# Performance work log

Hardware: AMD Instinct MI355X
Metric: run time of the kernel (lower is better)

The kernel has to match this reference:

```python
import jax, jax.numpy as jnp
import numpy as np

EPS = 1e-8
NUM_GCN_LAYERS = 2


def _cos(a, b):
    # cosine similarity along last axis, torch.nn.CosineSimilarity semantics
    num = jnp.sum(a * b, axis=-1)
    den = jnp.maximum(jnp.linalg.norm(a, axis=-1) * jnp.linalg.norm(b, axis=-1), EPS)
    return num / den


def _masked_mean(x, mask):
    # x: [..., L, D], mask: [..., L]
    s = jnp.sum(x * mask[..., None], axis=-2)
    d = jnp.maximum(jnp.sum(mask, axis=-1, keepdims=True), 1.0)
    return s / d


def setup_inputs() -> dict:
    key = jax.random.key(0)
    ks = jax.random.split(key, 12)
    B, C, L, D, P, OM, OE, R = 32, 16, 128, 768, 196, 10, 10, 36
    return {
        "mention_text_feature": jax.random.normal(ks[0], (B, L, D), jnp.float32),
        "mention_text_mask": jnp.ones((B, L), jnp.float32),
        "mention_start_pos": jax.random.randint(ks[1], (B,), 0, L),
        "mention_end_pos": jax.random.randint(ks[2], (B,), 0, L),
        "mention_image_feature": jax.random.normal(ks[3], (B, P, D), jnp.float32),
        "mention_object_feature": jax.random.normal(ks[4], (B, OM, R, D), jnp.float32),
        "mention_object_score": jax.random.uniform(ks[5], (B, OM), jnp.float32, 0.1, 1.0),
        "entity_text_feature": jax.random.normal(ks[6], (B, C, L, D), jnp.float32),
        "entity_text_mask": jnp.ones((B, C, L), jnp.float32),
        "entity_image_feature": jax.random.normal(ks[7], (B, C, P, D), jnp.float32),
        "entity_object_feature": jax.random.normal(ks[8], (B, C, OE, R, D), jnp.float32),
        "entity_object_score": jax.random.uniform(ks[9], (B, C, OE), jnp.float32, 0.1, 1.0),
        "miet_similarity": jax.random.normal(ks[10], (B, C), jnp.float32),
        "mtei_similarity": jax.random.normal(ks[11], (B, C), jnp.float32),
    }


def _forward(mtf, mtm, msp, mep, mif, mof, mos, etf, etm, eif, eof, eos, miet, mtei):
    B, L, D = mtf.shape
    C = etf.shape[1]

    # ---- VertexEncoder ----
    v_mt = _masked_mean(mtf, mtm)      # [B, D] mention text vertex
    v_mi = jnp.mean(mif, axis=-2)      # [B, D] mention image vertex
    v_et = _masked_mean(etf, etm)      # [B, C, D] entity text vertex
    v_ei = jnp.mean(eif, axis=-2)      # [B, C, D] entity image vertex

    # ---- EdgeEncoder ----
    # mention final repr: mean of start/end token features (span boundary repr)
    start = jnp.take_along_axis(mtf, msp[:, None, None], axis=1)[:, 0]  # [B, D]
    end = jnp.take_along_axis(mtf, mep[:, None, None], axis=1)[:, 0]    # [B, D]
    m_span = 0.5 * (start + end)
    mtet = _cos(m_span[:, None, :], etf[:, :, 0])  # [B, C] vs entity CLS token

    # miei: the original double python loop over (i, j) object pairs is a
    # weighted average of pairwise cosine sims -> one fused einsum pass.
    m = jnp.mean(mof, axis=-2)         # [B, OM, D]
    e = jnp.mean(eof, axis=-2)         # [B, C, OE, D]
    mn = m / jnp.maximum(jnp.linalg.norm(m, axis=-1, keepdims=True), EPS)
    en = e / jnp.maximum(jnp.linalg.norm(e, axis=-1, keepdims=True), EPS)
    cos_ij = jnp.einsum('bid,bcjd->bcij', mn, en)          # [B, C, OM, OE]
    w = mos[:, None, :, None] * eos[:, :, None, :]          # [B, C, OM, OE]
    miei = jnp.sum(cos_ij * w, axis=(2, 3)) / jnp.sum(w, axis=(2, 3))  # [B, C]

    # ---- GCN layers ----
    edges = [jnp.broadcast_to(x[:, :, None], (B, C, D)) for x in (mtet, mtei, miet, miei)]
    vertexes = [v_mt, v_mi, v_et, v_ei]
    vertex_graph = [[(0, 2), (1, 3)], [(2, 2), (3, 3)], [(0, 0), (2, 1)], [(1, 0), (3, 1)]]
    edge_graph = [(0, 2), (0, 3), (1, 2), (1, 3)]

    def conv_v(edge, v, mention_like):
        msg = edge * (v[:, None, :] if v.ndim == 2 else v)  # [B, C, D]
        return jnp.mean(msg, axis=1) if mention_like else msg

    def conv_e(u, v):
        u2 = u[:, None, :] if u.ndim == 2 else u
        v2 = v[:, None, :] if v.ndim == 2 else v
        return u2 * v2  # [B, C, D]

    for _ in range(NUM_GCN_LAYERS):
        new_v = []
        for k, nbrs in enumerate(vertex_graph):
            mention_like = k < 2  # vertexes 0,1 are [B,D]; 2,3 are [B,C,D]
            acc = conv_v(edges[nbrs[0][0]], vertexes[nbrs[0][1]], mention_like)
            acc = acc + conv_v(edges[nbrs[1][0]], vertexes[nbrs[1][1]], mention_like)
            new_v.append(acc)
        new_e = [conv_e(vertexes[ui], vertexes[vi]) for ui, vi in edge_graph]
        vertexes, edges = new_v, new_e

    mention, entity = vertexes[0], vertexes[2]
    return _cos(mention[:, None, :], entity)  # [B, C]


def reference(mention_text_feature, mention_text_mask, mention_start_pos, mention_end_pos, mention_image_feature, mention_object_feature, mention_object_score, entity_text_feature, entity_text_mask, entity_image_feature, entity_object_feature, entity_object_score, miet_similarity, mtei_similarity):
    return _forward(mention_text_feature, mention_text_mask, mention_start_pos, mention_end_pos, mention_image_feature, mention_object_feature, mention_object_score, entity_text_feature, entity_text_mask, entity_image_feature, entity_object_feature, entity_object_score, miet_similarity, mtei_similarity)
```

## Files before the change

### kernel.cpp

```cpp
#include <hip/hip_runtime.h>

#define EPSF 1e-8f

#define B_  32
#define C_  16
#define L_  128
#define D_  768
#define D4_ 192
#define P_  196
#define OM_ 10
#define OE_ 10
#define R_  36

__device__ __forceinline__ float4 f4add(float4 a, float4 b){
  return make_float4(a.x+b.x, a.y+b.y, a.z+b.z, a.w+b.w);
}
__device__ __forceinline__ float4 f4scale(float4 a, float s){
  return make_float4(a.x*s, a.y*s, a.z*s, a.w*s);
}
__device__ __forceinline__ float f4dot(float4 a, float4 b){
  return a.x*b.x + a.y*b.y + a.z*b.z + a.w*b.w;
}
__device__ __forceinline__ float wave_sum(float v){
  #pragma unroll
  for (int off = 32; off > 0; off >>= 1) v += __shfl_down(v, off);
  return v;
}

__global__ __launch_bounds__(192)
void means_k(const float* __restrict__ eif, const float* __restrict__ etf,
             const float* __restrict__ mof, const float* __restrict__ mif,
             const float* __restrict__ mtf,
             const float* __restrict__ etm, const float* __restrict__ mtm,
             float* __restrict__ part_eif, float* __restrict__ part_etf,
             float* __restrict__ part_mof, float* __restrict__ part_mif,
             float* __restrict__ part_mtf, float* __restrict__ msum)
{
  int blk = blockIdx.x;
  const float* in; const float* mask = nullptr;
  float* part; float* ms = nullptr;
  int ROWS, CH, RPC;
  if (blk < 3584)      { in = eif; part = part_eif; ROWS = 196; CH = 7; RPC = 28; }
  else if (blk < 5632) { blk -= 3584; in = etf; mask = etm; ms = msum + 128;
                         part = part_etf; ROWS = 128; CH = 4; RPC = 32; }
  else if (blk < 6272) { blk -= 5632; in = mof; part = part_mof; ROWS = 36; CH = 2; RPC = 18; }
  else if (blk < 6496) { blk -= 6272; in = mif; part = part_mif; ROWS = 196; CH = 7; RPC = 28; }
  else                 { blk -= 6496; in = mtf; mask = mtm; ms = msum;
                         part = part_mtf; ROWS = 128; CH = 4; RPC = 32; }

  int g = blk / CH, ch = blk - g * CH;
  int r0 = ch * RPC;
  int r1 = r0 + RPC; if (r1 > ROWS) r1 = ROWS;
  int t = threadIdx.x;
  const float4* inp = (const float4*)in + (size_t)g * ROWS * D4_;
  float4 acc = make_float4(0.f, 0.f, 0.f, 0.f);
  if (mask) {
    const float* mrow = mask + (size_t)g * ROWS;
    float msacc = 0.f;
    #pragma unroll 4
    for (int r = r0; r < r1; ++r) {
      float w = mrow[r];
      float4 v = inp[(size_t)r * D4_ + t];
      acc.x += v.x * w; acc.y += v.y * w; acc.z += v.z * w; acc.w += v.w * w;
      msacc += w;
    }
    if (t == 0) ms[blk] = msacc;
  } else {
    #pragma unroll 4
    for (int r = r0; r < r1; ++r)
      acc = f4add(acc, inp[(size_t)r * D4_ + t]);
  }
  ((float4*)part)[(size_t)blk * D4_ + t] = acc;
}

__device__ __forceinline__ void combine_body(const float* __restrict__ part,
                                             const float* __restrict__ msum,
                                             float* __restrict__ out,
                                             int secblk, int CH, float invn)
{
  int idx = secblk * 256 + threadIdx.x;
  int g = idx / D4_, t = idx - g * D4_;
  const float4* pp = (const float4*)part + (size_t)(g * CH) * D4_ + t;
  float4 acc = make_float4(0.f, 0.f, 0.f, 0.f);
  for (int ch = 0; ch < CH; ++ch) acc = f4add(acc, pp[(size_t)ch * D4_]);
  float scale;
  if (msum) {
    float s = 0.f;
    for (int ch = 0; ch < CH; ++ch) s += msum[g * CH + ch];
    scale = 1.f / fmaxf(s, 1.f);
  } else scale = invn;
  ((float4*)out)[idx] = f4scale(acc, scale);
}

__global__ __launch_bounds__(256)
void combine_k(const float* __restrict__ part_eif, const float* __restrict__ part_etf,
               const float* __restrict__ part_mof, const float* __restrict__ part_mif,
               const float* __restrict__ part_mtf, const float* __restrict__ msum,
               const float* __restrict__ etf, const float* __restrict__ mtf,
               const int* __restrict__ msp, const int* __restrict__ mep,
               const float* __restrict__ mos,
               float* __restrict__ v_ei, float* __restrict__ v_et,
               float* __restrict__ m_mean, float* __restrict__ v_mi,
               float* __restrict__ v_mt, float* __restrict__ q,
               float* __restrict__ mtet)
{
  int blk = blockIdx.x;
  if (blk < 384)       { combine_body(part_eif, nullptr, v_ei, blk, 7, 1.f/196.f); return; }
  else if (blk < 768)  { combine_body(part_etf, msum + 128, v_et, blk - 384, 4, 0.f); return; }
  else if (blk < 1008) { combine_body(part_mof, nullptr, m_mean, blk - 768, 2, 1.f/36.f); return; }
  else if (blk < 1032) { combine_body(part_mif, nullptr, v_mi, blk - 1008, 7, 1.f/196.f); return; }
  else if (blk < 1056) { combine_body(part_mtf, msum, v_mt, blk - 1032, 4, 0.f); return; }
  else if (blk < 1136) {
    int w = (blk - 1056) * 4 + (threadIdx.x >> 6);
    int lane = threadIdx.x & 63;
    const float4* pm = (const float4*)part_mof + (size_t)(w * 2) * D4_;
    const float inv36 = 1.f / 36.f;
    float n = 0.f;
    #pragma unroll
    for (int k = 0; k < 3; ++k) {
      float4 v = f4scale(f4add(pm[lane + 64*k], pm[(size_t)D4_ + lane + 64*k]), inv36);
      n += f4dot(v, v);
    }
    n = wave_sum(n);
    if (lane == 0) q[w] = mos[w] / fmaxf(sqrtf(n), EPSF);
    return;
  } else {
    int w = (blk - 1136) * 4 + (threadIdx.x >> 6);
    int lane = threadIdx.x & 63;
    int b = w >> 4;
    const float4* ecls = (const float4*)etf + (size_t)w * L_ * D4_;
    const float4* mb   = (const float4*)mtf + (size_t)b * L_ * D4_;
    int sp = msp[b], ep = mep[b];
    float dt = 0.f, na = 0.f, nb = 0.f;
    #pragma unroll
    for (int k = 0; k < 3; ++k) {
      float4 a = f4scale(f4add(mb[(size_t)sp * D4_ + lane + 64*k],
                               mb[(size_t)ep * D4_ + lane + 64*k]), 0.5f);
      float4 e = ecls[lane + 64*k];
      dt += f4dot(a, e); na += f4dot(a, a); nb += f4dot(e, e);
    }
    dt = wave_sum(dt); na = wave_sum(na); nb = wave_sum(nb);
    if (lane == 0) mtet[w] = dt / fmaxf(sqrtf(na) * sqrtf(nb), EPSF);
  }
}

__global__ __launch_bounds__(128)
void eof_dot_k(const float* __restrict__ eof, const float* __restrict__ m_mean,
               const float* __restrict__ q, const float* __restrict__ eos,
               float* __restrict__ p)
{
  int blk = blockIdx.x;
  int bc = blk / 5, jp = blk - bc * 5;
  int b = bc / C_;
  int wave = threadIdx.x >> 6, lane = threadIdx.x & 63;
  int j = jp * 2 + wave;
  size_t g = (size_t)bc * OE_ + j;
  const float4* ep = (const float4*)eof + g * R_ * D4_;
  float4 a0 = make_float4(0,0,0,0), a1 = a0, a2 = a0;
  #pragma unroll 4
  for (int r = 0; r < R_; ++r) {
    const float4* row = ep + (size_t)r * D4_;
    a0 = f4add(a0, row[lane]);
    a1 = f4add(a1, row[lane + 64]);
    a2 = f4add(a2, row[lane + 128]);
  }
  const float inv36 = 1.f / 36.f;
  a0 = f4scale(a0, inv36); a1 = f4scale(a1, inv36); a2 = f4scale(a2, inv36);
  float nrm = f4dot(a0, a0) + f4dot(a1, a1) + f4dot(a2, a2);
  float s = 0.f;
  const float4* mp = (const float4*)m_mean + (size_t)b * OM_ * D4_;
  #pragma unroll
  for (int i = 0; i < OM_; ++i) {
    const float4* mr = mp + (size_t)i * D4_;
    float di = f4dot(a0, mr[lane]) + f4dot(a1, mr[lane + 64]) + f4dot(a2, mr[lane + 128]);
    s += q[b * OM_ + i] * di;
  }
  s = wave_sum(s); nrm = wave_sum(nrm);
  if (lane == 0) {
    float einv = 1.f / fmaxf(sqrtf(nrm), EPSF);
    p[g] = eos[g] * s * einv;
  }
}

__global__ __launch_bounds__(256)
void tail_k(const float* __restrict__ p, const float* __restrict__ mos,
            const float* __restrict__ eos,
            const float* __restrict__ v_mt, const float* __restrict__ v_mi,
            const float* __restrict__ v_et, const float* __restrict__ v_ei,
            const float* __restrict__ mtet, const float* __restrict__ mtei,
            const float* __restrict__ miet,
            float* __restrict__ out)
{
  __shared__ float sh_e0[C_], sh_e1[C_], sh_e2[C_], sh_e3[C_];
  __shared__ float4 sh_m4[D4_], sh_s4[D4_];
  int b = blockIdx.x, tid = threadIdx.x;

  if (tid < C_) {
    int bc = b * C_ + tid;
    float num = 0.f, se = 0.f, sm = 0.f;
    #pragma unroll
    for (int j = 0; j < OE_; ++j) { num += p[bc * OE_ + j]; se += eos[bc * OE_ + j]; }
    #pragma unroll
    for (int i = 0; i < OM_; ++i) sm += mos[b * OM_ + i];
    sh_e3[tid] = num / (sm * se);
    sh_e0[tid] = mtet[bc];
    sh_e1[tid] = mtei[bc];
    sh_e2[tid] = miet[bc];
  }
  __syncthreads();

  const float invC = 1.f / (float)C_;
  for (int d = tid; d < D_; d += 256) {
    float vmt = v_mt[b * D_ + d], vmi = v_mi[b * D_ + d];
    float nv0 = 0.f, nv1 = 0.f, macc = 0.f;
    #pragma unroll
    for (int c = 0; c < C_; ++c) {
      int bc = b * C_ + c;
      float et = v_et[(size_t)bc * D_ + d];
      float ei = v_ei[(size_t)bc * D_ + d];
      float e0 = sh_e0[c], e1 = sh_e1[c], e2 = sh_e2[c], e3 = sh_e3[c];
      nv0 += e0 * et + e1 * ei;
      nv1 += e2 * et + e3 * ei;
      macc += (vmt * et) * (e0 * vmt + e2 * vmi)
            + (vmt * ei) * (e1 * vmt + e3 * vmi);
    }
    ((float*)sh_m4)[d] = macc * invC;
    ((float*)sh_s4)[d] = vmt * (nv0 * invC) + vmi * (nv1 * invC);
  }
  __syncthreads();

  int wv = tid >> 6, lane = tid & 63;
  for (int c = wv; c < C_; c += 4) {
    const float4* ep = (const float4*)v_et + (size_t)(b * C_ + c) * D4_;
    float dt = 0.f, nm = 0.f, ne = 0.f;
    #pragma unroll
    for (int k = 0; k < 3; ++k) {
      float4 m = sh_m4[lane + 64*k];
      float4 sv = sh_s4[lane + 64*k];
      float4 e = ep[lane + 64*k];
      float4 ent = make_float4(e.x * sv.x, e.y * sv.y, e.z * sv.z, e.w * sv.w);
      dt += f4dot(m, ent); nm += f4dot(m, m); ne += f4dot(ent, ent);
    }
    dt = wave_sum(dt); nm = wave_sum(nm); ne = wave_sum(ne);
    if (lane == 0) out[b * C_ + c] = dt / fmaxf(sqrtf(nm) * sqrtf(ne), EPSF);
  }
}

extern "C" void kernel_launch(void* const* d_in, const int* in_sizes, int n_in,
                              void* d_out, int out_size, void* d_ws, size_t ws_size,
                              hipStream_t stream)
{
  const float* mtf  = (const float*)d_in[0];
  const float* mtm  = (const float*)d_in[1];
  const int*   msp  = (const int*)  d_in[2];
  const int*   mep  = (const int*)  d_in[3];
  const float* mif  = (const float*)d_in[4];
  const float* mof  = (const float*)d_in[5];
  const float* mos  = (const float*)d_in[6];
  const float* etf  = (const float*)d_in[7];
  const float* etm  = (const float*)d_in[8];
  const float* eif  = (const float*)d_in[9];
  const float* eofp = (const float*)d_in[10];
  const float* eos  = (const float*)d_in[11];
  const float* miet = (const float*)d_in[12];
  const float* mtei = (const float*)d_in[13];
  float* out = (float*)d_out;
  float* ws = (float*)d_ws;

  float* PART_EIF = ws;
  float* PART_ETF = PART_EIF + 2752512;
  float* PART_MOF = PART_ETF + 1572864;
  float* PART_MIF = PART_MOF + 491520;
  float* PART_MTF = PART_MIF + 172032;
  float* MSUM     = PART_MTF + 98304;
  float* V_MT     = MSUM     + 2560;
  float* V_MI     = V_MT     + 24576;
  float* V_ET     = V_MI     + 24576;
  float* V_EI     = V_ET     + 393216;
  float* M_MEAN   = V_EI     + 393216;
  float* Q        = M_MEAN   + 245760;
  float* MTET     = Q        + 512;
  float* P_BUF    = MTET     + 512;

  means_k<<<6624, 192, 0, stream>>>(eif, etf, mof, mif, mtf, etm, mtm,
                                    PART_EIF, PART_ETF, PART_MOF, PART_MIF,
                                    PART_MTF, MSUM);

  combine_k<<<1264, 256, 0, stream>>>(PART_EIF, PART_ETF, PART_MOF, PART_MIF,
                                      PART_MTF, MSUM, etf, mtf, msp, mep, mos,
                                      V_EI, V_ET, M_MEAN, V_MI, V_MT, Q, MTET);

  eof_dot_k<<<B_ * C_ * 5, 128, 0, stream>>>(eofp, M_MEAN, Q, eos, P_BUF);

  tail_k<<<B_, 256, 0, stream>>>(P_BUF, mos, eos, V_MT, V_MI, V_ET, V_EI,
                                 MTET, mtei, miet, out);
}
```

Before: 229.7 us.

## Fold entity-object means into main reduction and precombine mention object vector

The per-object reduction over the entity object features now happens in the big means kernel, with each block writing a mean row to a new e_bar buffer. The separate eof_dot kernel therefore no longer serializes that bandwidth-heavy stream after combine. The weighted sum over mention objects is factored into one vector per batch (mq = sum q_i * m_i), so the final dot is one D-length product per entity object instead of ten. This adds an intermediate buffer of about 15 MB that is written and read back. It also reorders the floating-point summation slightly.

After: 243.3 us. 5.9% more time.

```diff
diff --git a/kernel.cpp b/kernel.cpp
--- a/kernel.cpp
+++ b/kernel.cpp
@@ -28,30 +28,42 @@
 }
 
 __global__ __launch_bounds__(192)
-void means_k(const float* __restrict__ eif, const float* __restrict__ etf,
-             const float* __restrict__ mof, const float* __restrict__ mif,
-             const float* __restrict__ mtf,
-             const float* __restrict__ etm, const float* __restrict__ mtm,
-             float* __restrict__ part_eif, float* __restrict__ part_etf,
-             float* __restrict__ part_mof, float* __restrict__ part_mif,
-             float* __restrict__ part_mtf, float* __restrict__ msum)
+void mega_k(const float* __restrict__ eofp, const float* __restrict__ eif,
+            const float* __restrict__ etf, const float* __restrict__ mof,
+            const float* __restrict__ mif, const float* __restrict__ mtf,
+            const float* __restrict__ etm, const float* __restrict__ mtm,
+            float* __restrict__ e_bar,
+            float* __restrict__ part_eif, float* __restrict__ part_etf,
+            float* __restrict__ part_mof, float* __restrict__ part_mif,
+            float* __restrict__ part_mtf, float* __restrict__ msum)
 {
   int blk = blockIdx.x;
+  int t = threadIdx.x;
+
+  if (blk < 5120) {
+    const float4* ep = (const float4*)eofp + (size_t)blk * R_ * D4_;
+    float4 acc = make_float4(0.f, 0.f, 0.f, 0.f);
+    #pragma unroll 6
+    for (int r = 0; r < R_; ++r)
+      acc = f4add(acc, ep[(size_t)r * D4_ + t]);
+    ((float4*)e_bar)[(size_t)blk * D4_ + t] = f4scale(acc, 1.f / 36.f);
+    return;
+  }
+
   const float* in; const float* mask = nullptr;
   float* part; float* ms = nullptr;
   int ROWS, CH, RPC;
-  if (blk < 3584)      { in = eif; part = part_eif; ROWS = 196; CH = 7; RPC = 28; }
-  else if (blk < 5632) { blk -= 3584; in = etf; mask = etm; ms = msum + 128;
-                         part = part_etf; ROWS = 128; CH = 4; RPC = 32; }
-  else if (blk < 6272) { blk -= 5632; in = mof; part = part_mof; ROWS = 36; CH = 2; RPC = 18; }
-  else if (blk < 6496) { blk -= 6272; in = mif; part = part_mif; ROWS = 196; CH = 7; RPC = 28; }
-  else                 { blk -= 6496; in = mtf; mask = mtm; ms = msum;
-                         part = part_mtf; ROWS = 128; CH = 4; RPC = 32; }
+  if (blk < 8704)       { blk -= 5120; in = eif; part = part_eif; ROWS = 196; CH = 7; RPC = 28; }
+  else if (blk < 10752) { blk -= 8704; in = etf; mask = etm; ms = msum + 128;
+                          part = part_etf; ROWS = 128; CH = 4; RPC = 32; }
+  else if (blk < 11392) { blk -= 10752; in = mof; part = part_mof; ROWS = 36; CH = 2; RPC = 18; }
+  else if (blk < 11616) { blk -= 11392; in = mif; part = part_mif; ROWS = 196; CH = 7; RPC = 28; }
+  else                  { blk -= 11616; in = mtf; mask = mtm; ms = msum;
+                          part = part_mtf; ROWS = 128; CH = 4; RPC = 32; }
 
   int g = blk / CH, ch = blk - g * CH;
   int r0 = ch * RPC;
   int r1 = r0 + RPC; if (r1 > ROWS) r1 = ROWS;
-  int t = threadIdx.x;
   const float4* inp = (const float4*)in + (size_t)g * ROWS * D4_;
   float4 acc = make_float4(0.f, 0.f, 0.f, 0.f);
   if (mask) {
@@ -93,39 +105,53 @@
 }
 
 __global__ __launch_bounds__(256)
-void combine_k(const float* __restrict__ part_eif, const float* __restrict__ part_etf,
-               const float* __restrict__ part_mof, const float* __restrict__ part_mif,
-               const float* __restrict__ part_mtf, const float* __restrict__ msum,
-               const float* __restrict__ etf, const float* __restrict__ mtf,
-               const int* __restrict__ msp, const int* __restrict__ mep,
-               const float* __restrict__ mos,
-               float* __restrict__ v_ei, float* __restrict__ v_et,
-               float* __restrict__ m_mean, float* __restrict__ v_mi,
-               float* __restrict__ v_mt, float* __restrict__ q,
-               float* __restrict__ mtet)
+void comb_k(const float* __restrict__ part_eif, const float* __restrict__ part_etf,
+            const float* __restrict__ part_mof, const float* __restrict__ part_mif,
+            const float* __restrict__ part_mtf, const float* __restrict__ msum,
+            const float* __restrict__ etf, const float* __restrict__ mtf,
+            const int* __restrict__ msp, const int* __restrict__ mep,
+            const float* __restrict__ mos,
+            float* __restrict__ v_ei, float* __restrict__ v_et,
+            float* __restrict__ v_mi, float* __restrict__ v_mt,
+            float* __restrict__ mq, float* __restrict__ mtet)
 {
   int blk = blockIdx.x;
   if (blk < 384)       { combine_body(part_eif, nullptr, v_ei, blk, 7, 1.f/196.f); return; }
   else if (blk < 768)  { combine_body(part_etf, msum + 128, v_et, blk - 384, 4, 0.f); return; }
-  else if (blk < 1008) { combine_body(part_mof, nullptr, m_mean, blk - 768, 2, 1.f/36.f); return; }
-  else if (blk < 1032) { combine_body(part_mif, nullptr, v_mi, blk - 1008, 7, 1.f/196.f); return; }
-  else if (blk < 1056) { combine_body(part_mtf, msum, v_mt, blk - 1032, 4, 0.f); return; }
-  else if (blk < 1136) {
-    int w = (blk - 1056) * 4 + (threadIdx.x >> 6);
-    int lane = threadIdx.x & 63;
-    const float4* pm = (const float4*)part_mof + (size_t)(w * 2) * D4_;
+  else if (blk < 792)  { combine_body(part_mif, nullptr, v_mi, blk - 768, 7, 1.f/196.f); return; }
+  else if (blk < 816)  { combine_body(part_mtf, msum, v_mt, blk - 792, 4, 0.f); return; }
+  else if (blk < 848) {
+    __shared__ float sh_n[4][OM_];
+    int b = blk - 816;
+    int tid = threadIdx.x, wv = tid >> 6, lane = tid & 63;
+    int t = tid;
+    bool act = (t < D4_);
+    float4 m[OM_];
+    const float4* pm = (const float4*)part_mof + (size_t)(b * OM_ * 2) * D4_;
     const float inv36 = 1.f / 36.f;
-    float n = 0.f;
-    #pragma unroll
-    for (int k = 0; k < 3; ++k) {
-      float4 v = f4scale(f4add(pm[lane + 64*k], pm[(size_t)D4_ + lane + 64*k]), inv36);
-      n += f4dot(v, v);
-    }
-    n = wave_sum(n);
-    if (lane == 0) q[w] = mos[w] / fmaxf(sqrtf(n), EPSF);
+    #pragma unroll
+    for (int i = 0; i < OM_; ++i) {
+      float4 v = make_float4(0.f, 0.f, 0.f, 0.f);
+      if (act) v = f4scale(f4add(pm[(size_t)(2*i) * D4_ + t],
+                                 pm[(size_t)(2*i+1) * D4_ + t]), inv36);
+      m[i] = v;
+      float n = wave_sum(f4dot(v, v));
+      if (lane == 0) sh_n[wv][i] = n;
+    }
+    __syncthreads();
+    if (act) {
+      float4 acc = make_float4(0.f, 0.f, 0.f, 0.f);
+      #pragma unroll
+      for (int i = 0; i < OM_; ++i) {
+        float nrm = sh_n[0][i] + sh_n[1][i] + sh_n[2][i] + sh_n[3][i];
+        float qi = mos[b * OM_ + i] / fmaxf(sqrtf(nrm), EPSF);
+        acc = f4add(acc, f4scale(m[i], qi));
+      }
+      ((float4*)mq)[b * D4_ + t] = acc;
+    }
     return;
   } else {
-    int w = (blk - 1136) * 4 + (threadIdx.x >> 6);
+    int w = (blk - 848) * 4 + (threadIdx.x >> 6);
     int lane = threadIdx.x & 63;
     int b = w >> 4;
     const float4* ecls = (const float4*)etf + (size_t)w * L_ * D4_;
@@ -144,42 +170,24 @@
   }
 }
 
-__global__ __launch_bounds__(128)
-void eof_dot_k(const float* __restrict__ eof, const float* __restrict__ m_mean,
-               const float* __restrict__ q, const float* __restrict__ eos,
-               float* __restrict__ p)
-{
-  int blk = blockIdx.x;
-  int bc = blk / 5, jp = blk - bc * 5;
-  int b = bc / C_;
-  int wave = threadIdx.x >> 6, lane = threadIdx.x & 63;
-  int j = jp * 2 + wave;
-  size_t g = (size_t)bc * OE_ + j;
-  const float4* ep = (const float4*)eof + g * R_ * D4_;
-  float4 a0 = make_float4(0,0,0,0), a1 = a0, a2 = a0;
-  #pragma unroll 4
-  for (int r = 0; r < R_; ++r) {
-    const float4* row = ep + (size_t)r * D4_;
-    a0 = f4add(a0, row[lane]);
-    a1 = f4add(a1, row[lane + 64]);
-    a2 = f4add(a2, row[lane + 128]);
-  }
-  const float inv36 = 1.f / 36.f;
-  a0 = f4scale(a0, inv36); a1 = f4scale(a1, inv36); a2 = f4scale(a2, inv36);
-  float nrm = f4dot(a0, a0) + f4dot(a1, a1) + f4dot(a2, a2);
-  float s = 0.f;
-  const float4* mp = (const float4*)m_mean + (size_t)b * OM_ * D4_;
+__global__ __launch_bounds__(256)
+void p_k(const float* __restrict__ e_bar, const float* __restrict__ mq,
+         const float* __restrict__ eos, float* __restrict__ p)
+{
+  int g = blockIdx.x * 4 + (threadIdx.x >> 6);
+  int lane = threadIdx.x & 63;
+  int b = g / (C_ * OE_);
+  const float4* ep = (const float4*)e_bar + (size_t)g * D4_;
+  const float4* mp = (const float4*)mq + (size_t)b * D4_;
+  float dt = 0.f, ne = 0.f;
   #pragma unroll
-  for (int i = 0; i < OM_; ++i) {
-    const float4* mr = mp + (size_t)i * D4_;
-    float di = f4dot(a0, mr[lane]) + f4dot(a1, mr[lane + 64]) + f4dot(a2, mr[lane + 128]);
-    s += q[b * OM_ + i] * di;
-  }
-  s = wave_sum(s); nrm = wave_sum(nrm);
-  if (lane == 0) {
-    float einv = 1.f / fmaxf(sqrtf(nrm), EPSF);
-    p[g] = eos[g] * s * einv;
-  }
+  for (int k = 0; k < 3; ++k) {
+    float4 e = ep[lane + 64*k];
+    float4 m = mp[lane + 64*k];
+    dt += f4dot(m, e); ne += f4dot(e, e);
+  }
+  dt = wave_sum(dt); ne = wave_sum(ne);
+  if (lane == 0) p[g] = eos[g] * dt / fmaxf(sqrtf(ne), EPSF);
 }
 
 __global__ __launch_bounds__(256)
@@ -267,30 +275,30 @@
   float* out = (float*)d_out;
   float* ws = (float*)d_ws;
 
-  float* PART_EIF = ws;
+  float* E_BAR    = ws;
+  float* PART_EIF = E_BAR    + 3932160;
   float* PART_ETF = PART_EIF + 2752512;
   float* PART_MOF = PART_ETF + 1572864;
   float* PART_MIF = PART_MOF + 491520;
   float* PART_MTF = PART_MIF + 172032;
   float* MSUM     = PART_MTF + 98304;
-  float* V_MT     = MSUM     + 2560;
+  float* V_MT     = MSUM     + 2176;
   float* V_MI     = V_MT     + 24576;
   float* V_ET     = V_MI     + 24576;
   float* V_EI     = V_ET     + 393216;
-  float* M_MEAN   = V_EI     + 393216;
-  float* Q        = M_MEAN   + 245760;
-  float* MTET     = Q        + 512;
+  float* MQ       = V_EI     + 393216;
+  float* MTET     = MQ       + 24576;
   float* P_BUF    = MTET     + 512;
 
-  means_k<<<6624, 192, 0, stream>>>(eif, etf, mof, mif, mtf, etm, mtm,
-                                    PART_EIF, PART_ETF, PART_MOF, PART_MIF,
-                                    PART_MTF, MSUM);
-
-  combine_k<<<1264, 256, 0, stream>>>(PART_EIF, PART_ETF, PART_MOF, PART_MIF,
-                                      PART_MTF, MSUM, etf, mtf, msp, mep, mos,
-                                      V_EI, V_ET, M_MEAN, V_MI, V_MT, Q, MTET);
-
-  eof_dot_k<<<B_ * C_ * 5, 128, 0, stream>>>(eofp, M_MEAN, Q, eos, P_BUF);
+  mega_k<<<11744, 192, 0, stream>>>(eofp, eif, etf, mof, mif, mtf, etm, mtm,
+                                    E_BAR, PART_EIF, PART_ETF, PART_MOF,
+                                    PART_MIF, PART_MTF, MSUM);
+
+  comb_k<<<976, 256, 0, stream>>>(PART_EIF, PART_ETF, PART_MOF, PART_MIF,
+                                  PART_MTF, MSUM, etf, mtf, msp, mep, mos,
+                                  V_EI, V_ET, V_MI, V_MT, MQ, MTET);
+
+  p_k<<<1280, 256, 0, stream>>>(E_BAR, MQ, eos, P_BUF);
 
   tail_k<<<B_, 256, 0, stream>>>(P_BUF, mos, eos, V_MT, V_MI, V_ET, V_EI,
                                  MTET, mtei, miet, out);
```

## Compute mention object means first and fuse entity object dots into mean pass

Applied to the files above, without the earlier changes.

A small mof_k kernel now computes the mention object means and their inverse-norm weights up front. The entity-object reduction and dot product is folded into the big means kernel as extra blocks, so the bandwidth-heavy streams of entity objects, entity images and entity text share one launch instead of two serialized ones. The partial-sum path for mention objects and its combine step are removed. This trades one large launch boundary for a small dependency kernel at the start, and the entity-object blocks now run three waves per block.

Result: no change. 226.0 us (-1.6%).

```diff
diff --git a/kernel.cpp b/kernel.cpp
--- a/kernel.cpp
+++ b/kernel.cpp
@@ -28,30 +28,83 @@
 }
 
 __global__ __launch_bounds__(192)
-void means_k(const float* __restrict__ eif, const float* __restrict__ etf,
-             const float* __restrict__ mof, const float* __restrict__ mif,
+void mof_k(const float* __restrict__ mof, const float* __restrict__ mos,
+           float* __restrict__ m_mean, float* __restrict__ q)
+{
+  int blk = blockIdx.x;
+  int t = threadIdx.x, wv = t >> 6, lane = t & 63;
+  const float4* inp = (const float4*)mof + (size_t)blk * R_ * D4_;
+  float4 acc = make_float4(0.f, 0.f, 0.f, 0.f);
+  #pragma unroll 6
+  for (int r = 0; r < R_; ++r)
+    acc = f4add(acc, inp[(size_t)r * D4_ + t]);
+  acc = f4scale(acc, 1.f / 36.f);
+  ((float4*)m_mean)[(size_t)blk * D4_ + t] = acc;
+  __shared__ float sh[3];
+  float n = wave_sum(f4dot(acc, acc));
+  if (lane == 0) sh[wv] = n;
+  __syncthreads();
+  if (t == 0) q[blk] = mos[blk] / fmaxf(sqrtf(sh[0] + sh[1] + sh[2]), EPSF);
+}
+
+__global__ __launch_bounds__(192)
+void mega2_k(const float* __restrict__ eofp, const float* __restrict__ eif,
+             const float* __restrict__ etf, const float* __restrict__ mif,
              const float* __restrict__ mtf,
              const float* __restrict__ etm, const float* __restrict__ mtm,
+             const float* __restrict__ m_mean, const float* __restrict__ q,
+             const float* __restrict__ eos,
              float* __restrict__ part_eif, float* __restrict__ part_etf,
-             float* __restrict__ part_mof, float* __restrict__ part_mif,
-             float* __restrict__ part_mtf, float* __restrict__ msum)
+             float* __restrict__ part_mif, float* __restrict__ part_mtf,
+             float* __restrict__ msum, float* __restrict__ p)
 {
   int blk = blockIdx.x;
+  int t = threadIdx.x;
+
+  if (blk < 1707) {
+    int wave = t >> 6, lane = t & 63;
+    int g = blk * 3 + wave;
+    if (g >= 5120) return;
+    int b = g / (C_ * OE_);
+    const float4* ep = (const float4*)eofp + (size_t)g * R_ * D4_;
+    float4 a0 = make_float4(0,0,0,0), a1 = a0, a2 = a0;
+    #pragma unroll 4
+    for (int r = 0; r < R_; ++r) {
+      const float4* row = ep + (size_t)r * D4_;
+      a0 = f4add(a0, row[lane]);
+      a1 = f4add(a1, row[lane + 64]);
+      a2 = f4add(a2, row[lane + 128]);
+    }
+    const float inv36 = 1.f / 36.f;
+    a0 = f4scale(a0, inv36); a1 = f4scale(a1, inv36); a2 = f4scale(a2, inv36);
+    float nrm = f4dot(a0, a0) + f4dot(a1, a1) + f4dot(a2, a2);
+    float s = 0.f;
+    const float4* mp = (const float4*)m_mean + (size_t)b * OM_ * D4_;
+    #pragma unroll
+    for (int i = 0; i < OM_; ++i) {
+      const float4* mr = mp + (size_t)i * D4_;
+      float di = f4dot(a0, mr[lane]) + f4dot(a1, mr[lane + 64]) + f4dot(a2, mr[lane + 128]);
+      s += q[b * OM_ + i] * di;
+    }
+    s = wave_sum(s); nrm = wave_sum(nrm);
+    if (lane == 0) p[g] = eos[g] * s / fmaxf(sqrtf(nrm), EPSF);
+    return;
+  }
+
+  blk -= 1707;
   const float* in; const float* mask = nullptr;
   float* part; float* ms = nullptr;
   int ROWS, CH, RPC;
   if (blk < 3584)      { in = eif; part = part_eif; ROWS = 196; CH = 7; RPC = 28; }
   else if (blk < 5632) { blk -= 3584; in = etf; mask = etm; ms = msum + 128;
                          part = part_etf; ROWS = 128; CH = 4; RPC = 32; }
-  else if (blk < 6272) { blk -= 5632; in = mof; part = part_mof; ROWS = 36; CH = 2; RPC = 18; }
-  else if (blk < 6496) { blk -= 6272; in = mif; part = part_mif; ROWS = 196; CH = 7; RPC = 28; }
-  else                 { blk -= 6496; in = mtf; mask = mtm; ms = msum;
+  else if (blk < 5856) { blk -= 5632; in = mif; part = part_mif; ROWS = 196; CH = 7; RPC = 28; }
+  else                 { blk -= 5856; in = mtf; mask = mtm; ms = msum;
                          part = part_mtf; ROWS = 128; CH = 4; RPC = 32; }
 
   int g = blk / CH, ch = blk - g * CH;
   int r0 = ch * RPC;
   int r1 = r0 + RPC; if (r1 > ROWS) r1 = ROWS;
-  int t = threadIdx.x;
   const float4* inp = (const float4*)in + (size_t)g * ROWS * D4_;
   float4 acc = make_float4(0.f, 0.f, 0.f, 0.f);
   if (mask) {
@@ -93,39 +146,22 @@
 }
 
 __global__ __launch_bounds__(256)
-void combine_k(const float* __restrict__ part_eif, const float* __restrict__ part_etf,
-               const float* __restrict__ part_mof, const float* __restrict__ part_mif,
-               const float* __restrict__ part_mtf, const float* __restrict__ msum,
-               const float* __restrict__ etf, const float* __restrict__ mtf,
-               const int* __restrict__ msp, const int* __restrict__ mep,
-               const float* __restrict__ mos,
-               float* __restrict__ v_ei, float* __restrict__ v_et,
-               float* __restrict__ m_mean, float* __restrict__ v_mi,
-               float* __restrict__ v_mt, float* __restrict__ q,
-               float* __restrict__ mtet)
+void comb2_k(const float* __restrict__ part_eif, const float* __restrict__ part_etf,
+             const float* __restrict__ part_mif, const float* __restrict__ part_mtf,
+             const float* __restrict__ msum,
+             const float* __restrict__ etf, const float* __restrict__ mtf,
+             const int* __restrict__ msp, const int* __restrict__ mep,
+             float* __restrict__ v_ei, float* __restrict__ v_et,
+             float* __restrict__ v_mi, float* __restrict__ v_mt,
+             float* __restrict__ mtet)
 {
   int blk = blockIdx.x;
   if (blk < 384)       { combine_body(part_eif, nullptr, v_ei, blk, 7, 1.f/196.f); return; }
   else if (blk < 768)  { combine_body(part_etf, msum + 128, v_et, blk - 384, 4, 0.f); return; }
-  else if (blk < 1008) { combine_body(part_mof, nullptr, m_mean, blk - 768, 2, 1.f/36.f); return; }
-  else if (blk < 1032) { combine_body(part_mif, nullptr, v_mi, blk - 1008, 7, 1.f/196.f); return; }
-  else if (blk < 1056) { combine_body(part_mtf, msum, v_mt, blk - 1032, 4, 0.f); return; }
-  else if (blk < 1136) {
-    int w = (blk - 1056) * 4 + (threadIdx.x >> 6);
-    int lane = threadIdx.x & 63;
-    const float4* pm = (const float4*)part_mof + (size_t)(w * 2) * D4_;
-    const float inv36 = 1.f / 36.f;
-    float n = 0.f;
-    #pragma unroll
-    for (int k = 0; k < 3; ++k) {
-      float4 v = f4scale(f4add(pm[lane + 64*k], pm[(size_t)D4_ + lane + 64*k]), inv36);
-      n += f4dot(v, v);
-    }
-    n = wave_sum(n);
-    if (lane == 0) q[w] = mos[w] / fmaxf(sqrtf(n), EPSF);
-    return;
-  } else {
-    int w = (blk - 1136) * 4 + (threadIdx.x >> 6);
+  else if (blk < 792)  { combine_body(part_mif, nullptr, v_mi, blk - 768, 7, 1.f/196.f); return; }
+  else if (blk < 816)  { combine_body(part_mtf, msum, v_mt, blk - 792, 4, 0.f); return; }
+  else {
+    int w = (blk - 816) * 4 + (threadIdx.x >> 6);
     int lane = threadIdx.x & 63;
     int b = w >> 4;
     const float4* ecls = (const float4*)etf + (size_t)w * L_ * D4_;
@@ -141,44 +177,6 @@
     }
     dt = wave_sum(dt); na = wave_sum(na); nb = wave_sum(nb);
     if (lane == 0) mtet[w] = dt / fmaxf(sqrtf(na) * sqrtf(nb), EPSF);
-  }
-}
-
-__global__ __launch_bounds__(128)
-void eof_dot_k(const float* __restrict__ eof, const float* __restrict__ m_mean,
-               const float* __restrict__ q, const float* __restrict__ eos,
-               float* __restrict__ p)
-{
-  int blk = blockIdx.x;
-  int bc = blk / 5, jp = blk - bc * 5;
-  int b = bc / C_;
-  int wave = threadIdx.x >> 6, lane = threadIdx.x & 63;
-  int j = jp * 2 + wave;
-  size_t g = (size_t)bc * OE_ + j;
-  const float4* ep = (const float4*)eof + g * R_ * D4_;
-  float4 a0 = make_float4(0,0,0,0), a1 = a0, a2 = a0;
-  #pragma unroll 4
-  for (int r = 0; r < R_; ++r) {
-    const float4* row = ep + (size_t)r * D4_;
-    a0 = f4add(a0, row[lane]);
-    a1 = f4add(a1, row[lane + 64]);
-    a2 = f4add(a2, row[lane + 128]);
-  }
-  const float inv36 = 1.f / 36.f;
-  a0 = f4scale(a0, inv36); a1 = f4scale(a1, inv36); a2 = f4scale(a2, inv36);
-  float nrm = f4dot(a0, a0) + f4dot(a1, a1) + f4dot(a2, a2);
-  float s = 0.f;
-  const float4* mp = (const float4*)m_mean + (size_t)b * OM_ * D4_;
-  #pragma unroll
-  for (int i = 0; i < OM_; ++i) {
-    const float4* mr = mp + (size_t)i * D4_;
-    float di = f4dot(a0, mr[lane]) + f4dot(a1, mr[lane + 64]) + f4dot(a2, mr[lane + 128]);
-    s += q[b * OM_ + i] * di;
-  }
-  s = wave_sum(s); nrm = wave_sum(nrm);
-  if (lane == 0) {
-    float einv = 1.f / fmaxf(sqrtf(nrm), EPSF);
-    p[g] = eos[g] * s * einv;
   }
 }
 
@@ -269,28 +267,28 @@
 
   float* PART_EIF = ws;
   float* PART_ETF = PART_EIF + 2752512;
-  float* PART_MOF = PART_ETF + 1572864;
-  float* PART_MIF = PART_MOF + 491520;
+  float* PART_MIF = PART_ETF + 1572864;
   float* PART_MTF = PART_MIF + 172032;
   float* MSUM     = PART_MTF + 98304;
-  float* V_MT     = MSUM     + 2560;
+  float* M_MEAN   = MSUM     + 2176;
+  float* Q        = M_MEAN   + 245760;
+  float* V_MT     = Q        + 512;
   float* V_MI     = V_MT     + 24576;
   float* V_ET     = V_MI     + 24576;
   float* V_EI     = V_ET     + 393216;
-  float* M_MEAN   = V_EI     + 393216;
-  float* Q        = M_MEAN   + 245760;
-  float* MTET     = Q        + 512;
+  float* MTET     = V_EI     + 393216;
   float* P_BUF    = MTET     + 512;
 
-  means_k<<<6624, 192, 0, stream>>>(eif, etf, mof, mif, mtf, etm, mtm,
-                                    PART_EIF, PART_ETF, PART_MOF, PART_MIF,
-                                    PART_MTF, MSUM);
-
-  combine_k<<<1264, 256, 0, stream>>>(PART_EIF, PART_ETF, PART_MOF, PART_MIF,
-                                      PART_MTF, MSUM, etf, mtf, msp, mep, mos,
-                                      V_EI, V_ET, M_MEAN, V_MI, V_MT, Q, MTET);
-
-  eof_dot_k<<<B_ * C_ * 5, 128, 0, stream>>>(eofp, M_MEAN, Q, eos, P_BUF);
+  mof_k<<<320, 192, 0, stream>>>(mof, mos, M_MEAN, Q);
+
+  mega2_k<<<7691, 192, 0, stream>>>(eofp, eif, etf, mif, mtf, etm, mtm,
+                                    M_MEAN, Q, eos,
+                                    PART_EIF, PART_ETF, PART_MIF, PART_MTF,
+                                    MSUM, P_BUF);
+
+  comb2_k<<<944, 256, 0, stream>>>(PART_EIF, PART_ETF, PART_MIF, PART_MTF,
+                                   MSUM, etf, mtf, msp, mep,
+                                   V_EI, V_ET, V_MI, V_MT, MTET);
 
   tail_k<<<B_, 256, 0, stream>>>(P_BUF, mos, eos, V_MT, V_MI, V_ET, V_EI,
                                  MTET, mtei, miet, out);
```
